# Kernel optimization log

Measured on AMD Instinct MI355X. Metric: run time of the kernel, lower is better.

Reference implementation:

```python
import jax, jax.numpy as jnp
import numpy as np

D_MODEL = 1024
DK = 64
N_HEADS = D_MODEL // DK
MASK = True


def setup_inputs() -> dict:
    key = jax.random.key(0)
    ks = jax.random.split(key, 8)
    B, S = 4, 2048
    scale = 1.0 / np.sqrt(D_MODEL)
    return {
        "query_data": jax.random.normal(ks[0], (B, S, D_MODEL), dtype=jnp.float32),
        "key_data": jax.random.normal(ks[1], (B, S, D_MODEL), dtype=jnp.float32),
        "value_data": jax.random.normal(ks[2], (B, S, D_MODEL), dtype=jnp.float32),
        "Wq": jax.random.normal(ks[3], (D_MODEL, D_MODEL), dtype=jnp.float32) * scale,
        "Wk": jax.random.normal(ks[4], (D_MODEL, D_MODEL), dtype=jnp.float32) * scale,
        "Wv": jax.random.normal(ks[5], (D_MODEL, D_MODEL), dtype=jnp.float32) * scale,
        "Wp": jax.random.normal(ks[6], (D_MODEL, D_MODEL), dtype=jnp.float32) * scale,
        "bp": jnp.zeros((D_MODEL,), dtype=jnp.float32),
    }


def reference(query_data, key_data, value_data, Wq, Wk, Wv, Wp, bp):
    B, S, _ = query_data.shape
    # QKV projections, split into heads: (B, H, S, dk)
    def split_heads(x, W):
        return (x @ W.T).reshape(B, -1, N_HEADS, DK).transpose(0, 2, 1, 3)

    q = split_heads(query_data, Wq)
    k = split_heads(key_data, Wk)
    v = split_heads(value_data, Wv)

    scores = jnp.einsum("bhqd,bhkd->bhqk", q, k) / np.sqrt(DK).astype(np.float32)
    if MASK:
        Sq, Sk = scores.shape[-2], scores.shape[-1]
        causal = jnp.triu(jnp.ones((Sq, Sk), dtype=scores.dtype), k=1) * jnp.float32(-1e13)
        scores = scores + causal  # broadcast over (B, H)
    attn = jax.nn.softmax(scores, axis=-1)
    out = jnp.einsum("bhqk,bhkd->bhqd", attn, v)
    out = out.transpose(0, 2, 1, 3).reshape(B, S, D_MODEL)
    # dropout is identity in eval mode
    return out @ Wp.T + bp
```

## Files before the change

kernel.cpp:

```cpp
#include <hip/hip_runtime.h>
#include <hip/hip_bf16.h>
#include <stdint.h>

#define D_MODEL 1024
#define SEQ     2048
#define BATCH   4
#define NH      16
#define DKK     64
#define MROWS   (BATCH * SEQ)

typedef unsigned short u16;
using bf16x8 = __attribute__((ext_vector_type(8))) __bf16;
using f32x4  = __attribute__((ext_vector_type(4))) float;

__device__ __forceinline__ u16 f2bf(float f) {
    union { float f; uint32_t u; } v; v.f = f;
    return (u16)((v.u + 0x7FFFu + ((v.u >> 16) & 1u)) >> 16);
}
__device__ __forceinline__ uint32_t pk2bf(float a, float b) {
    union { __hip_bfloat162 h; uint32_t u; } v;
    v.h = __float22bfloat162_rn(float2{a, b});
    return v.u;
}

__device__ __forceinline__ float fast_exp2(float x) {
    float r; asm("v_exp_f32 %0, %1" : "=v"(r) : "v"(x)); return r;
}
__device__ __forceinline__ float fast_rcp(float x) {
    float r; asm("v_rcp_f32 %0, %1" : "=v"(r) : "v"(x)); return r;
}

__device__ __forceinline__ void gl_lds16(const u16* g, u16* l) {
    __builtin_amdgcn_global_load_lds(
        (__attribute__((address_space(1))) void*)(const_cast<u16*>(g)),
        (__attribute__((address_space(3))) void*)l, 16, 0, 0);
}

__device__ __forceinline__ int swz(int o, int n) {
    const int pos = ((n >> 3) ^ (o & 15)) ^ (((o >> 4) & 1) << 2);
    return o * 128 + (pos << 3) + (n & 7);
}
__device__ __forceinline__ int swzg(int o, int gn) {
    const int pos = (gn ^ (o & 15)) ^ (((o >> 4) & 1) << 2);
    return o * 128 + (pos << 3);
}

__global__ __launch_bounds__(256) void cvt_all(const float* __restrict__ a,
                                               const float* __restrict__ b,
                                               const float* __restrict__ c,
                                               const float* __restrict__ wq,
                                               const float* __restrict__ wk,
                                               const float* __restrict__ wv,
                                               const float* __restrict__ wp,
                                               u16* __restrict__ da, u16* __restrict__ db,
                                               u16* __restrict__ dc, u16* __restrict__ dq,
                                               u16* __restrict__ dk, u16* __restrict__ dv,
                                               u16* __restrict__ dp) {
    const int i = blockIdx.x * 256 + threadIdx.x;
    const float* s; u16* d; int off;
    if (i < 3 * (1 << 21)) {
        const int sel = i >> 21; off = i & ((1 << 21) - 1);
        s = (sel == 0) ? a : (sel == 1) ? b : c;
        d = (sel == 0) ? da : (sel == 1) ? db : dc;
    } else {
        const int j = i - 3 * (1 << 21);
        const int sel = j >> 18; off = j & ((1 << 18) - 1);
        s = (sel == 0) ? wq : (sel == 1) ? wk : (sel == 2) ? wv : wp;
        d = (sel == 0) ? dq : (sel == 1) ? dk : (sel == 2) ? dv : dp;
    }
    float4 v = ((const float4*)s)[off];
    uint2 o;
    o.x = pk2bf(v.x, v.y); o.y = pk2bf(v.z, v.w);
    ((uint2*)d)[off] = o;
}

__global__ __launch_bounds__(256, 3) void gemm_qkv(const u16* __restrict__ XQ,
                                                   const u16* __restrict__ XK,
                                                   const u16* __restrict__ XV,
                                                   const u16* __restrict__ WQ,
                                                   const u16* __restrict__ WK,
                                                   const u16* __restrict__ WV,
                                                   u16* __restrict__ Qo,
                                                   u16* __restrict__ Ko,
                                                   u16* __restrict__ Vto) {
    constexpr int K = 1024, N = 1024;
    __shared__ __align__(16) u16 smem[16384];
    u16* ldsA = smem;
    u16* ldsB = smem + 8192;
    u16* ldsT = smem;

    const int which = blockIdx.x >> 9;
    const int inner = blockIdx.x & 511;
    const u16* A  = (which == 0) ? XQ : (which == 1) ? XK : XV;
    const u16* Bw = (which == 0) ? WQ : (which == 1) ? WK : WV;

    const int t = threadIdx.x;
    const int w = t >> 6, lane = t & 63;
    const int quad = lane >> 4, l15 = lane & 15;
    const int x = inner & 7, j = inner >> 3;
    const int bm = x * 8 + (j >> 3), bn = j & 7;
    const int wm = (w >> 1) * 64, wn = (w & 1) * 64;

    const u16* Ab = A  + (size_t)bm * 128 * K;
    const u16* Bb = Bw + (size_t)bn * 128 * K;
    const int srow  = lane >> 2;
    const int scol8 = (lane & 3) * 8;

    f32x4 acc[4][4];
    #pragma unroll
    for (int i = 0; i < 4; ++i)
        #pragma unroll
        for (int jj = 0; jj < 4; ++jj)
            acc[i][jj] = f32x4{0.f, 0.f, 0.f, 0.f};

    #pragma unroll
    for (int i = 0; i < 2; ++i) {
        const int c = w * 2 + i;
        gl_lds16(Ab + (size_t)(c * 16 + srow) * K + scol8, &ldsA[c * 512]);
        gl_lds16(Bb + (size_t)(c * 16 + srow) * K + scol8, &ldsB[c * 512]);
    }

    int cur = 0;
    for (int k0 = 0; k0 < K; k0 += 32) {
        __syncthreads();
        if (k0 + 32 < K) {
            const int nxt = cur ^ 1;
            #pragma unroll
            for (int i = 0; i < 2; ++i) {
                const int c = w * 2 + i;
                gl_lds16(Ab + (size_t)(c * 16 + srow) * K + k0 + 32 + scol8, &ldsA[nxt * 4096 + c * 512]);
                gl_lds16(Bb + (size_t)(c * 16 + srow) * K + k0 + 32 + scol8, &ldsB[nxt * 4096 + c * 512]);
            }
        }

        bf16x8 afr[4], bfr[4];
        #pragma unroll
        for (int i = 0; i < 4; ++i)
            afr[i] = *(const bf16x8*)&ldsA[cur * 4096 + (wm + i * 16 + l15) * 32 + quad * 8];
        #pragma unroll
        for (int jj = 0; jj < 4; ++jj)
            bfr[jj] = *(const bf16x8*)&ldsB[cur * 4096 + (wn + jj * 16 + l15) * 32 + quad * 8];

        #pragma unroll
        for (int i = 0; i < 4; ++i)
            #pragma unroll
            for (int jj = 0; jj < 4; ++jj)
                acc[i][jj] = __builtin_amdgcn_mfma_f32_16x16x32_bf16(afr[i], bfr[jj], acc[i][jj], 0, 0, 0);
        cur ^= 1;
    }

    __syncthreads();

    if (which < 2) {
        u16* outb = which ? Ko : Qo;
        #pragma unroll
        for (int i = 0; i < 4; ++i)
            #pragma unroll
            for (int jj = 0; jj < 4; ++jj)
                #pragma unroll
                for (int r = 0; r < 4; ++r)
                    ldsT[swz(wm + i * 16 + quad * 4 + r, wn + jj * 16 + l15)] = f2bf(acc[i][jj][r]);
        __syncthreads();
        const int rr = t >> 1, half = t & 1;
        u16* dstg = outb + (size_t)(bm * 128 + rr) * N + bn * 128;
        #pragma unroll
        for (int k = 0; k < 8; ++k) {
            const int gn = half * 8 + k;
            *(uint4*)(dstg + gn * 8) = *(const uint4*)&ldsT[swzg(rr, gn)];
        }
    } else {
        #pragma unroll
        for (int i = 0; i < 4; ++i)
            #pragma unroll
            for (int jj = 0; jj < 4; ++jj)
                #pragma unroll
                for (int r = 0; r < 4; ++r)
                    ldsT[swz(wn + jj * 16 + l15, wm + i * 16 + quad * 4 + r)] = f2bf(acc[i][jj][r]);
        __syncthreads();
        const int c = t >> 1, half = t & 1;
        const int colg = bn * 128 + c;
        const int hh = colg >> 6, dd = colg & 63;
        const int bb = bm >> 4;
        const int s0 = (bm * 128) & 2047;
        u16* dstg = Vto + (size_t)((bb * NH + hh) * DKK + dd) * SEQ + s0;
        #pragma unroll
        for (int k = 0; k < 8; ++k) {
            const int gn = half * 8 + k;
            *(uint4*)(dstg + gn * 8) = *(const uint4*)&ldsT[swzg(c, gn)];
        }
    }
}

__global__ __launch_bounds__(256, 4) void gemm_proj(const u16* __restrict__ A,
                                                    const u16* __restrict__ Bw,
                                                    float* __restrict__ outf,
                                                    const float* __restrict__ bias) {
    constexpr int K = 1024, N = 1024;
    __shared__ __align__(16) u16 ldsA[2 * 2048];
    __shared__ __align__(16) u16 ldsB[2 * 4096];

    const int t = threadIdx.x;
    const int w = t >> 6, lane = t & 63;
    const int quad = lane >> 4, l15 = lane & 15;
    const int x = blockIdx.x & 7, j = blockIdx.x >> 3;
    const int bm = x * 16 + (j >> 3), bn = j & 7;
    const int wm = (w >> 1) * 32, wn = (w & 1) * 64;

    const u16* Ab = A  + (size_t)bm * 64 * K;
    const u16* Bb = Bw + (size_t)bn * 128 * K;
    const int srow  = lane >> 2;
    const int scol8 = (lane & 3) * 8;

    f32x4 acc[2][4];
    #pragma unroll
    for (int i = 0; i < 2; ++i)
        #pragma unroll
        for (int jj = 0; jj < 4; ++jj)
            acc[i][jj] = f32x4{0.f, 0.f, 0.f, 0.f};

    gl_lds16(Ab + (size_t)(w * 16 + srow) * K + scol8, &ldsA[w * 512]);
    #pragma unroll
    for (int i = 0; i < 2; ++i) {
        const int c = w * 2 + i;
        gl_lds16(Bb + (size_t)(c * 16 + srow) * K + scol8, &ldsB[c * 512]);
    }

    int cur = 0;
    for (int k0 = 0; k0 < K; k0 += 32) {
        __syncthreads();
        if (k0 + 32 < K) {
            const int nxt = cur ^ 1;
            gl_lds16(Ab + (size_t)(w * 16 + srow) * K + k0 + 32 + scol8, &ldsA[nxt * 2048 + w * 512]);
            #pragma unroll
            for (int i = 0; i < 2; ++i) {
                const int c = w * 2 + i;
                gl_lds16(Bb + (size_t)(c * 16 + srow) * K + k0 + 32 + scol8, &ldsB[nxt * 4096 + c * 512]);
            }
        }

        bf16x8 afr[2], bfr[4];
        #pragma unroll
        for (int i = 0; i < 2; ++i)
            afr[i] = *(const bf16x8*)&ldsA[cur * 2048 + (wm + i * 16 + l15) * 32 + quad * 8];
        #pragma unroll
        for (int jj = 0; jj < 4; ++jj)
            bfr[jj] = *(const bf16x8*)&ldsB[cur * 4096 + (wn + jj * 16 + l15) * 32 + quad * 8];

        #pragma unroll
        for (int i = 0; i < 2; ++i)
            #pragma unroll
            for (int jj = 0; jj < 4; ++jj)
                acc[i][jj] = __builtin_amdgcn_mfma_f32_16x16x32_bf16(afr[i], bfr[jj], acc[i][jj], 0, 0, 0);
        cur ^= 1;
    }

    #pragma unroll
    for (int i = 0; i < 2; ++i)
        #pragma unroll
        for (int jj = 0; jj < 4; ++jj)
            #pragma unroll
            for (int r = 0; r < 4; ++r) {
                const int row = bm * 64 + wm + i * 16 + quad * 4 + r;
                const int col = bn * 128 + wn + jj * 16 + l15;
                outf[(size_t)row * N + col] = acc[i][jj][r] + bias[col];
            }
}

__global__ __launch_bounds__(256, 4) void flash_attn(const u16* __restrict__ Qb,
                                                     const u16* __restrict__ Kb,
                                                     const u16* __restrict__ Vt,
                                                     u16* __restrict__ O) {
    __shared__ __align__(16) u16 ldsK[2 * 4096];
    __shared__ __align__(16) u16 ldsV[2 * 4096];
    __shared__ __align__(16) u16 ldsP[4 * 1024];

    const int t = threadIdx.x;
    const int w = t >> 6, lane = t & 63;
    const int quad = lane >> 4, l15 = lane & 15;
    const int bh = blockIdx.x & 63;
    const int qt = 15 - (blockIdx.x >> 6);
    const int b = bh >> 4, h = bh & 15;
    const int q0 = qt * 128;
    const int qw = q0 + w * 32;

    const int srow  = lane >> 2;
    const int scol8 = (lane & 3) * 8;
    const size_t kbase = (size_t)b * SEQ * D_MODEL + h * DKK;
    const size_t vbase = (size_t)(bh * DKK) * SEQ;

    bf16x8 qf[2][2];
    #pragma unroll
    for (int g = 0; g < 2; ++g) {
        const u16* Qrow = Qb + (size_t)(b * SEQ + qw + g * 16 + l15) * D_MODEL + h * DKK;
        qf[g][0] = *(const bf16x8*)(Qrow + quad * 8);
        qf[g][1] = *(const bf16x8*)(Qrow + 32 + quad * 8);
    }

    f32x4 o_acc[2][4];
    #pragma unroll
    for (int g = 0; g < 2; ++g)
        #pragma unroll
        for (int nt = 0; nt < 4; ++nt) o_acc[g][nt] = f32x4{0.f, 0.f, 0.f, 0.f};
    float l_i[2] = {0.f, 0.f};

    const float C2 = 0.18033688f;
    u16* PwS = &ldsP[w * 1024];

    const int ntiles = 2 * qt + 2;

    #pragma unroll
    for (int i = 0; i < 2; ++i) {
        const int e = w * 2 + i, ch = e >> 2, rb = (e & 3) * 16;
        gl_lds16(Kb + kbase + (size_t)(rb + srow) * D_MODEL + ch * 32 + scol8,
                 &ldsK[ch * 2048 + rb * 32]);
        gl_lds16(Vt + vbase + (size_t)(rb + srow) * SEQ + ch * 32 + scol8,
                 &ldsV[ch * 2048 + rb * 32]);
    }

    int cur = 0;
    for (int it = 0; it < ntiles; ++it) {
        const int kb = it * 64;
        __syncthreads();

        if (it + 1 < ntiles) {
            const int nb = kb + 64, nxt = cur ^ 1;
            #pragma unroll
            for (int i = 0; i < 2; ++i) {
                const int e = w * 2 + i, ch = e >> 2, rb = (e & 3) * 16;
                gl_lds16(Kb + kbase + (size_t)(nb + rb + srow) * D_MODEL + ch * 32 + scol8,
                         &ldsK[nxt * 4096 + ch * 2048 + rb * 32]);
                gl_lds16(Vt + vbase + (size_t)(rb + srow) * SEQ + nb + ch * 32 + scol8,
                         &ldsV[nxt * 4096 + ch * 2048 + rb * 32]);
            }
        }

        if (kb <= qw + 31) {
            f32x4 sc[2][4];
            #pragma unroll
            for (int g = 0; g < 2; ++g)
                #pragma unroll
                for (int jt = 0; jt < 4; ++jt) sc[g][jt] = f32x4{0.f, 0.f, 0.f, 0.f};
            #pragma unroll
            for (int ks = 0; ks < 2; ++ks)
                #pragma unroll
                for (int jt = 0; jt < 4; ++jt) {
                    bf16x8 kf = *(const bf16x8*)&ldsK[cur * 4096 + ks * 2048 + (jt * 16 + l15) * 32 + quad * 8];
                    #pragma unroll
                    for (int g = 0; g < 2; ++g)
                        sc[g][jt] = __builtin_amdgcn_mfma_f32_16x16x32_bf16(kf, qf[g][ks], sc[g][jt], 0, 0, 0);
                }

            if (kb + 63 >= qw) {
                #pragma unroll
                for (int g = 0; g < 2; ++g)
                    #pragma unroll
                    for (int jt = 0; jt < 4; ++jt)
                        #pragma unroll
                        for (int r = 0; r < 4; ++r)
                            if (kb + jt * 16 + quad * 4 + r > qw + g * 16 + l15) sc[g][jt][r] = -3.0e38f;
            }

            #pragma unroll
            for (int g = 0; g < 2; ++g) {
                float tsum = 0.f;
                #pragma unroll
                for (int jt = 0; jt < 4; ++jt) {
                    float p[4];
                    #pragma unroll
                    for (int r = 0; r < 4; ++r) {
                        p[r] = fast_exp2(sc[g][jt][r] * C2);
                        tsum += p[r];
                    }
                    const int pos = (4 * jt + quad) ^ l15;
                    uint2 pk;
                    pk.x = pk2bf(p[0], p[1]);
                    pk.y = pk2bf(p[2], p[3]);
                    *(uint2*)&PwS[l15 * 64 + pos * 4] = pk;
                }
                tsum += __shfl_xor(tsum, 16);
                tsum += __shfl_xor(tsum, 32);
                l_i[g] += tsum;

                asm volatile("s_waitcnt lgkmcnt(0)" ::: "memory");

                #pragma unroll
                for (int ks = 0; ks < 2; ++ks) {
                    const int gg = 8 * ks + 2 * quad;
                    union { bf16x8 v; uint2 u[2]; } pu;
                    pu.u[0] = *(const uint2*)&PwS[l15 * 64 + ((gg) ^ l15) * 4];
                    pu.u[1] = *(const uint2*)&PwS[l15 * 64 + ((gg + 1) ^ l15) * 4];
                    #pragma unroll
                    for (int nt = 0; nt < 4; ++nt) {
                        bf16x8 vf = *(const bf16x8*)&ldsV[cur * 4096 + ks * 2048 + (nt * 16 + l15) * 32 + quad * 8];
                        o_acc[g][nt] = __builtin_amdgcn_mfma_f32_16x16x32_bf16(pu.v, vf, o_acc[g][nt], 0, 0, 0);
                    }
                }
            }
        }

        cur ^= 1;
    }

    #pragma unroll
    for (int g = 0; g < 2; ++g) {
        const float rli = fast_rcp(l_i[g]);
        float rl[4];
        #pragma unroll
        for (int r = 0; r < 4; ++r)
            rl[r] = __shfl(rli, (lane & 48) | (quad * 4 + r));
        #pragma unroll
        for (int nt = 0; nt < 4; ++nt)
            #pragma unroll
            for (int r = 0; r < 4; ++r) {
                const int qg = qw + g * 16 + quad * 4 + r;
                O[(size_t)(b * SEQ + qg) * D_MODEL + h * DKK + nt * 16 + l15] = f2bf(o_acc[g][nt][r] * rl[r]);
            }
    }
}

extern "C" void kernel_launch(void* const* d_in, const int* in_sizes, int n_in,
                              void* d_out, int out_size, void* d_ws, size_t ws_size,
                              hipStream_t stream) {
    const float* q_in = (const float*)d_in[0];
    const float* k_in = (const float*)d_in[1];
    const float* v_in = (const float*)d_in[2];
    const float* Wq   = (const float*)d_in[3];
    const float* Wk   = (const float*)d_in[4];
    const float* Wv   = (const float*)d_in[5];
    const float* Wp   = (const float*)d_in[6];
    const float* bp   = (const float*)d_in[7];
    float* out = (float*)d_out;

    char* ws = (char*)d_ws;
    u16* XQ  = (u16*)(ws + (size_t)0);
    u16* XK  = (u16*)(ws + ((size_t)16 << 20));
    u16* XV  = (u16*)(ws + ((size_t)32 << 20));
    u16* WQb = (u16*)(ws + ((size_t)48 << 20));
    u16* WKb = (u16*)(ws + ((size_t)50 << 20));
    u16* WVb = (u16*)(ws + ((size_t)52 << 20));
    u16* WPb = (u16*)(ws + ((size_t)54 << 20));
    u16* Qb  = (u16*)(ws + ((size_t)56 << 20));
    u16* Kb  = (u16*)(ws + ((size_t)72 << 20));
    u16* Vtb = (u16*)(ws + ((size_t)88 << 20));

    const int n4 = 3 * (1 << 21) + 4 * (1 << 18);
    cvt_all<<<n4 / 256, 256, 0, stream>>>(q_in, k_in, v_in, Wq, Wk, Wv, Wp,
                                          XQ, XK, XV, WQb, WKb, WVb, WPb);

    gemm_qkv<<<1536, 256, 0, stream>>>(XQ, XK, XV, WQb, WKb, WVb, Qb, Kb, Vtb);

    flash_attn<<<BATCH * NH * (SEQ / 128), 256, 0, stream>>>(Qb, Kb, Vtb, XQ);

    gemm_proj<<<1024, 256, 0, stream>>>(XQ, WPb, out, bp);
}
```

Baseline: 327.5 us.

## Swizzle LDS staging, batch P for both row groups, stage O via LDS

Applies an XOR swizzle to the LDS column placement in all three kernels (QKV gemm, projection gemm, flash attention) so fragment reads avoid bank conflicts. In flash attention, the P tile is doubled so both 16-row groups are written before a single lgkmcnt wait, and each V fragment load feeds two MFMAs. The output is staged through LDS so it can be written with 16-byte coalesced stores. Launch bounds drop from 4 to 3 waves' occupancy hint, and ldsP doubles, which trades occupancy for fewer waits and better reuse.

```diff
diff --git a/kernel.cpp b/kernel.cpp
--- a/kernel.cpp
+++ b/kernel.cpp
@@ -34,6 +34,13 @@
     __builtin_amdgcn_global_load_lds(
         (__attribute__((address_space(1))) void*)(const_cast<u16*>(g)),
         (__attribute__((address_space(3))) void*)l, 16, 0, 0);
+}
+
+__device__ __forceinline__ int stage_col8(int lane) {
+    return (((lane & 3) ^ ((lane >> 3) & 3)) * 8);
+}
+__device__ __forceinline__ int frag_off(int row, int quad, int l15) {
+    return row * 32 + ((quad ^ ((l15 >> 1) & 3)) * 8);
 }
 
 __device__ __forceinline__ int swz(int o, int n) {
@@ -104,7 +111,7 @@
     const u16* Ab = A  + (size_t)bm * 128 * K;
     const u16* Bb = Bw + (size_t)bn * 128 * K;
     const int srow  = lane >> 2;
-    const int scol8 = (lane & 3) * 8;
+    const int sc8   = stage_col8(lane);
 
     f32x4 acc[4][4];
     #pragma unroll
@@ -116,8 +123,8 @@
     #pragma unroll
     for (int i = 0; i < 2; ++i) {
         const int c = w * 2 + i;
-        gl_lds16(Ab + (size_t)(c * 16 + srow) * K + scol8, &ldsA[c * 512]);
-        gl_lds16(Bb + (size_t)(c * 16 + srow) * K + scol8, &ldsB[c * 512]);
+        gl_lds16(Ab + (size_t)(c * 16 + srow) * K + sc8, &ldsA[c * 512]);
+        gl_lds16(Bb + (size_t)(c * 16 + srow) * K + sc8, &ldsB[c * 512]);
     }
 
     int cur = 0;
@@ -128,18 +135,18 @@
             #pragma unroll
             for (int i = 0; i < 2; ++i) {
                 const int c = w * 2 + i;
-                gl_lds16(Ab + (size_t)(c * 16 + srow) * K + k0 + 32 + scol8, &ldsA[nxt * 4096 + c * 512]);
-                gl_lds16(Bb + (size_t)(c * 16 + srow) * K + k0 + 32 + scol8, &ldsB[nxt * 4096 + c * 512]);
+                gl_lds16(Ab + (size_t)(c * 16 + srow) * K + k0 + 32 + sc8, &ldsA[nxt * 4096 + c * 512]);
+                gl_lds16(Bb + (size_t)(c * 16 + srow) * K + k0 + 32 + sc8, &ldsB[nxt * 4096 + c * 512]);
             }
         }
 
         bf16x8 afr[4], bfr[4];
         #pragma unroll
         for (int i = 0; i < 4; ++i)
-            afr[i] = *(const bf16x8*)&ldsA[cur * 4096 + (wm + i * 16 + l15) * 32 + quad * 8];
+            afr[i] = *(const bf16x8*)&ldsA[cur * 4096 + frag_off(wm + i * 16 + l15, quad, l15)];
         #pragma unroll
         for (int jj = 0; jj < 4; ++jj)
-            bfr[jj] = *(const bf16x8*)&ldsB[cur * 4096 + (wn + jj * 16 + l15) * 32 + quad * 8];
+            bfr[jj] = *(const bf16x8*)&ldsB[cur * 4096 + frag_off(wn + jj * 16 + l15, quad, l15)];
 
         #pragma unroll
         for (int i = 0; i < 4; ++i)
@@ -209,7 +216,7 @@
     const u16* Ab = A  + (size_t)bm * 64 * K;
     const u16* Bb = Bw + (size_t)bn * 128 * K;
     const int srow  = lane >> 2;
-    const int scol8 = (lane & 3) * 8;
+    const int sc8   = stage_col8(lane);
 
     f32x4 acc[2][4];
     #pragma unroll
@@ -218,11 +225,11 @@
         for (int jj = 0; jj < 4; ++jj)
             acc[i][jj] = f32x4{0.f, 0.f, 0.f, 0.f};
 
-    gl_lds16(Ab + (size_t)(w * 16 + srow) * K + scol8, &ldsA[w * 512]);
+    gl_lds16(Ab + (size_t)(w * 16 + srow) * K + sc8, &ldsA[w * 512]);
     #pragma unroll
     for (int i = 0; i < 2; ++i) {
         const int c = w * 2 + i;
-        gl_lds16(Bb + (size_t)(c * 16 + srow) * K + scol8, &ldsB[c * 512]);
+        gl_lds16(Bb + (size_t)(c * 16 + srow) * K + sc8, &ldsB[c * 512]);
     }
 
     int cur = 0;
@@ -230,21 +237,21 @@
         __syncthreads();
         if (k0 + 32 < K) {
             const int nxt = cur ^ 1;
-            gl_lds16(Ab + (size_t)(w * 16 + srow) * K + k0 + 32 + scol8, &ldsA[nxt * 2048 + w * 512]);
+            gl_lds16(Ab + (size_t)(w * 16 + srow) * K + k0 + 32 + sc8, &ldsA[nxt * 2048 + w * 512]);
             #pragma unroll
             for (int i = 0; i < 2; ++i) {
                 const int c = w * 2 + i;
-                gl_lds16(Bb + (size_t)(c * 16 + srow) * K + k0 + 32 + scol8, &ldsB[nxt * 4096 + c * 512]);
+                gl_lds16(Bb + (size_t)(c * 16 + srow) * K + k0 + 32 + sc8, &ldsB[nxt * 4096 + c * 512]);
             }
         }
 
         bf16x8 afr[2], bfr[4];
         #pragma unroll
         for (int i = 0; i < 2; ++i)
-            afr[i] = *(const bf16x8*)&ldsA[cur * 2048 + (wm + i * 16 + l15) * 32 + quad * 8];
+            afr[i] = *(const bf16x8*)&ldsA[cur * 2048 + frag_off(wm + i * 16 + l15, quad, l15)];
         #pragma unroll
         for (int jj = 0; jj < 4; ++jj)
-            bfr[jj] = *(const bf16x8*)&ldsB[cur * 4096 + (wn + jj * 16 + l15) * 32 + quad * 8];
+            bfr[jj] = *(const bf16x8*)&ldsB[cur * 4096 + frag_off(wn + jj * 16 + l15, quad, l15)];
 
         #pragma unroll
         for (int i = 0; i < 2; ++i)
@@ -266,13 +273,13 @@
             }
 }
 
-__global__ __launch_bounds__(256, 4) void flash_attn(const u16* __restrict__ Qb,
+__global__ __launch_bounds__(256, 3) void flash_attn(const u16* __restrict__ Qb,
                                                      const u16* __restrict__ Kb,
                                                      const u16* __restrict__ Vt,
                                                      u16* __restrict__ O) {
     __shared__ __align__(16) u16 ldsK[2 * 4096];
     __shared__ __align__(16) u16 ldsV[2 * 4096];
-    __shared__ __align__(16) u16 ldsP[4 * 1024];
+    __shared__ __align__(16) u16 ldsP[4 * 2048];
 
     const int t = threadIdx.x;
     const int w = t >> 6, lane = t & 63;
@@ -284,7 +291,7 @@
     const int qw = q0 + w * 32;
 
     const int srow  = lane >> 2;
-    const int scol8 = (lane & 3) * 8;
+    const int sc8   = stage_col8(lane);
     const size_t kbase = (size_t)b * SEQ * D_MODEL + h * DKK;
     const size_t vbase = (size_t)(bh * DKK) * SEQ;
 
@@ -304,16 +311,16 @@
     float l_i[2] = {0.f, 0.f};
 
     const float C2 = 0.18033688f;
-    u16* PwS = &ldsP[w * 1024];
+    u16* PwS = &ldsP[w * 2048];
 
     const int ntiles = 2 * qt + 2;
 
     #pragma unroll
     for (int i = 0; i < 2; ++i) {
         const int e = w * 2 + i, ch = e >> 2, rb = (e & 3) * 16;
-        gl_lds16(Kb + kbase + (size_t)(rb + srow) * D_MODEL + ch * 32 + scol8,
+        gl_lds16(Kb + kbase + (size_t)(rb + srow) * D_MODEL + ch * 32 + sc8,
                  &ldsK[ch * 2048 + rb * 32]);
-        gl_lds16(Vt + vbase + (size_t)(rb + srow) * SEQ + ch * 32 + scol8,
+        gl_lds16(Vt + vbase + (size_t)(rb + srow) * SEQ + ch * 32 + sc8,
                  &ldsV[ch * 2048 + rb * 32]);
     }
 
@@ -327,9 +334,9 @@
             #pragma unroll
             for (int i = 0; i < 2; ++i) {
                 const int e = w * 2 + i, ch = e >> 2, rb = (e & 3) * 16;
-                gl_lds16(Kb + kbase + (size_t)(nb + rb + srow) * D_MODEL + ch * 32 + scol8,
+                gl_lds16(Kb + kbase + (size_t)(nb + rb + srow) * D_MODEL + ch * 32 + sc8,
                          &ldsK[nxt * 4096 + ch * 2048 + rb * 32]);
-                gl_lds16(Vt + vbase + (size_t)(rb + srow) * SEQ + nb + ch * 32 + scol8,
+                gl_lds16(Vt + vbase + (size_t)(rb + srow) * SEQ + nb + ch * 32 + sc8,
                          &ldsV[nxt * 4096 + ch * 2048 + rb * 32]);
             }
         }
@@ -344,7 +351,7 @@
             for (int ks = 0; ks < 2; ++ks)
                 #pragma unroll
                 for (int jt = 0; jt < 4; ++jt) {
-                    bf16x8 kf = *(const bf16x8*)&ldsK[cur * 4096 + ks * 2048 + (jt * 16 + l15) * 32 + quad * 8];
+                    bf16x8 kf = *(const bf16x8*)&ldsK[cur * 4096 + ks * 2048 + frag_off(jt * 16 + l15, quad, l15)];
                     #pragma unroll
                     for (int g = 0; g < 2; ++g)
                         sc[g][jt] = __builtin_amdgcn_mfma_f32_16x16x32_bf16(kf, qf[g][ks], sc[g][jt], 0, 0, 0);
@@ -375,25 +382,30 @@
                     uint2 pk;
                     pk.x = pk2bf(p[0], p[1]);
                     pk.y = pk2bf(p[2], p[3]);
-                    *(uint2*)&PwS[l15 * 64 + pos * 4] = pk;
+                    *(uint2*)&PwS[g * 1024 + l15 * 64 + pos * 4] = pk;
                 }
                 tsum += __shfl_xor(tsum, 16);
                 tsum += __shfl_xor(tsum, 32);
                 l_i[g] += tsum;
-
-                asm volatile("s_waitcnt lgkmcnt(0)" ::: "memory");
-
-                #pragma unroll
-                for (int ks = 0; ks < 2; ++ks) {
-                    const int gg = 8 * ks + 2 * quad;
-                    union { bf16x8 v; uint2 u[2]; } pu;
-                    pu.u[0] = *(const uint2*)&PwS[l15 * 64 + ((gg) ^ l15) * 4];
-                    pu.u[1] = *(const uint2*)&PwS[l15 * 64 + ((gg + 1) ^ l15) * 4];
+            }
+
+            asm volatile("s_waitcnt lgkmcnt(0)" ::: "memory");
+
+            #pragma unroll
+            for (int ks = 0; ks < 2; ++ks) {
+                const int gg = 8 * ks + 2 * quad;
+                union { bf16x8 v; uint2 u[2]; } pu[2];
+                #pragma unroll
+                for (int g = 0; g < 2; ++g) {
+                    pu[g].u[0] = *(const uint2*)&PwS[g * 1024 + l15 * 64 + ((gg) ^ l15) * 4];
+                    pu[g].u[1] = *(const uint2*)&PwS[g * 1024 + l15 * 64 + ((gg + 1) ^ l15) * 4];
+                }
+                #pragma unroll
+                for (int nt = 0; nt < 4; ++nt) {
+                    bf16x8 vf = *(const bf16x8*)&ldsV[cur * 4096 + ks * 2048 + frag_off(nt * 16 + l15, quad, l15)];
                     #pragma unroll
-                    for (int nt = 0; nt < 4; ++nt) {
-                        bf16x8 vf = *(const bf16x8*)&ldsV[cur * 4096 + ks * 2048 + (nt * 16 + l15) * 32 + quad * 8];
-                        o_acc[g][nt] = __builtin_amdgcn_mfma_f32_16x16x32_bf16(pu.v, vf, o_acc[g][nt], 0, 0, 0);
-                    }
+                    for (int g = 0; g < 2; ++g)
+                        o_acc[g][nt] = __builtin_amdgcn_mfma_f32_16x16x32_bf16(pu[g].v, vf, o_acc[g][nt], 0, 0, 0);
                 }
             }
         }
@@ -401,6 +413,8 @@
         cur ^= 1;
     }
 
+    __syncthreads();
+    u16* ldsO = ldsK;
     #pragma unroll
     for (int g = 0; g < 2; ++g) {
         const float rli = fast_rcp(l_i[g]);
@@ -412,9 +426,16 @@
         for (int nt = 0; nt < 4; ++nt)
             #pragma unroll
             for (int r = 0; r < 4; ++r) {
-                const int qg = qw + g * 16 + quad * 4 + r;
-                O[(size_t)(b * SEQ + qg) * D_MODEL + h * DKK + nt * 16 + l15] = f2bf(o_acc[g][nt][r] * rl[r]);
-            }
+                const int row = w * 32 + g * 16 + quad * 4 + r;
+                ldsO[row * 64 + nt * 16 + l15] = f2bf(o_acc[g][nt][r] * rl[r]);
+            }
+    }
+    __syncthreads();
+    #pragma unroll
+    for (int it2 = 0; it2 < 4; ++it2) {
+        const int row = it2 * 32 + (t >> 3);
+        const uint4 v = *(const uint4*)&ldsO[row * 64 + (t & 7) * 8];
+        *(uint4*)(O + (size_t)(b * SEQ + q0 + row) * D_MODEL + h * DKK + (t & 7) * 8) = v;
     }
 }
 
```

Result: faster. 310.1 us (-5.3%).
